# Optimization experiments

Measured on AMD Instinct MI355X. Metric: run time of the kernel, lower is better.

Reference implementation:

```python
import jax, jax.numpy as jnp
import numpy as np

DIM = 1024
NUM_HEADS = 16
DIM_HEAD = 64
POOL = 8  # int(sqrt(agent_num=64))
SCALE = DIM_HEAD ** -0.5


def setup_inputs() -> dict:
    key = jax.random.key(0)
    k1, k2, k3, k4 = jax.random.split(key, 4)
    inner = NUM_HEADS * DIM_HEAD
    x = jax.random.normal(k1, (4, 4096, DIM), dtype=jnp.float32)
    # qkv Linear (no bias): weight stored as (in, out) so forward is x @ Wqkv
    Wqkv = jax.random.normal(k2, (DIM, 3 * inner), dtype=jnp.float32) * (DIM ** -0.5)
    Wo = jax.random.normal(k3, (inner, DIM), dtype=jnp.float32) * (inner ** -0.5)
    bo = jax.random.normal(k4, (DIM,), dtype=jnp.float32) * 0.01
    return {"x": x, "Wqkv": Wqkv, "Wo": Wo, "bo": bo}


def reference(x, Wqkv, Wo, bo):
    b, t, _ = x.shape
    h, d = NUM_HEADS, DIM_HEAD
    qkv = x @ Wqkv                                   # [b, t, 3*h*d]
    qkv = qkv.reshape(b, t, 3, h, d)                 # split (qkv h d)
    qkv = jnp.transpose(qkv, (2, 0, 3, 1, 4))        # [3, b, h, t, d]
    q, k, v = qkv[0], qkv[1], qkv[2]
    # AdaptiveAvgPool2d((POOL, d)) on [b,h,t,d]: identity on d, mean-pool t -> POOL
    # (t divisible by POOL -> exact reshape+mean)
    agent = q.reshape(b, h, POOL, t // POOL, d).mean(axis=3)  # [b, h, P, d]
    # stage 1: agents attend over keys, aggregate values
    s1 = jnp.einsum('bhid,bhjd->bhij', agent * SCALE, k)      # [b, h, P, t]
    p1 = jax.nn.softmax(s1, axis=-1)
    v_agent = jnp.einsum('bhij,bhjd->bhid', p1, v)            # [b, h, P, d]
    # stage 2: queries attend over agent tokens
    s2 = jnp.einsum('bhid,bhjd->bhij', q * SCALE, agent)      # [b, h, t, P]
    p2 = jax.nn.softmax(s2, axis=-1)
    out = jnp.einsum('bhij,bhjd->bhid', p2, v_agent)          # [b, h, t, d]
    out = jnp.transpose(out, (0, 2, 1, 3)).reshape(b, t, h * d)
    return out @ Wo + bo
```

## Files before the change

kernel.cpp:

```cpp
#include <hip/hip_runtime.h>
#include <hip/hip_bf16.h>
#include <stdint.h>

typedef __bf16 bf16;
typedef __attribute__((ext_vector_type(8))) __bf16 bf16x8;
typedef __attribute__((ext_vector_type(4))) float f32x4;
typedef __attribute__((ext_vector_type(4))) unsigned int u32x4;

#define NH 16
#define DH 64
#define POOL 8
#define BATCH 4
#define SEQ 4096
#define DIMV 1024
#define QKV_N (3*DIMV)
#define M_TOTAL (BATCH*SEQ)
#define SCALE_F 0.125f
#define AGS_F (SCALE_F / 512.0f)
#define BH (BATCH*NH)
#define TCH 16
#define TCL (SEQ/TCH)
#define HP 128

#define AS1(p) ((const __attribute__((address_space(1))) void*)(p))
#define AS3(p) ((__attribute__((address_space(3))) void*)(p))
typedef const __attribute__((address_space(3))) char* lds_cp;

__global__ void prep(const float* __restrict__ x, bf16* __restrict__ xb,
                     const float* __restrict__ Wqkv, bf16* __restrict__ WqkvT,
                     const float* __restrict__ Wo, bf16* __restrict__ WoT) {
  __shared__ float tile[32][33];
  const int b = blockIdx.x;
  if (b < 8192) {
    size_t i = ((size_t)b * 256 + threadIdx.x) * 8;
    float4 f0 = *(const float4*)(x + i);
    float4 f1 = *(const float4*)(x + i + 4);
    bf16x8 o;
    o[0] = (bf16)f0.x; o[1] = (bf16)f0.y; o[2] = (bf16)f0.z; o[3] = (bf16)f0.w;
    o[4] = (bf16)f1.x; o[5] = (bf16)f1.y; o[6] = (bf16)f1.z; o[7] = (bf16)f1.w;
    *(bf16x8*)(xb + i) = o;
    return;
  }
  const float* in; bf16* out; int C, bx, by;
  if (b < 9216) { int bb = b - 8192; in = Wqkv; out = WqkvT; C = QKV_N; bx = 64 + (bb & 31); by = bb >> 5; }
  else          { int bb = b - 9216; in = Wo;   out = WoT;   C = DIMV;  bx = bb & 31;        by = bb >> 5; }
  const int R = DIMV;
  int c0 = bx * 32, r0 = by * 32;
  int tx = threadIdx.x & 31, ty = threadIdx.x >> 5;
  for (int i = ty; i < 32; i += 8)
    tile[i][tx] = in[(size_t)(r0 + i) * C + c0 + tx];
  __syncthreads();
  for (int i = ty; i < 32; i += 8)
    out[(size_t)(c0 + i) * R + r0 + tx] = (bf16)tile[tx][i];
}

__global__ void pool_x(const bf16* __restrict__ xb, float* __restrict__ xpool) {
  const int bid = blockIdx.x;
  const int bucket = bid >> 3, slice = bid & 7;
  const int b = bucket >> 3, p = bucket & 7;
  const int tid = threadIdx.x;
  const int co = tid & 127;
  const int r0 = tid >> 7;
  const bf16* src = xb + ((size_t)b * SEQ + p * 512 + slice * 64 + r0) * DIMV + co * 8;
  float a[8] = {};
  for (int r = 0; r < 64; r += 2) {
    bf16x8 v = *(const bf16x8*)(src + (size_t)r * DIMV);
#pragma unroll
    for (int e = 0; e < 8; ++e) a[e] += (float)v[e];
  }
  float* dst = xpool + (size_t)bucket * DIMV + co * 8;
#pragma unroll
  for (int e = 0; e < 8; ++e) atomicAdd(&dst[e], a[e]);
}

__global__ void agent_build(const float* __restrict__ xpool, const float* __restrict__ Wqkv,
                            float* __restrict__ agent_s) {
  __shared__ float xp[256];
  const int bid = blockIdx.x;
  const int bp = bid >> 2, cs = bid & 3;
  const int tid = threadIdx.x;
  xp[tid] = xpool[(size_t)bp * DIMV + cs * 256 + tid];
  __syncthreads();
  float acc[4] = {};
  const float* wbase = Wqkv + (size_t)(cs * 256) * QKV_N + tid * 4;
#pragma unroll 8
  for (int c = 0; c < 256; ++c) {
    float xv = xp[c];
    float4 wv = *(const float4*)(wbase + (size_t)c * QKV_N);
    acc[0] += xv * wv.x; acc[1] += xv * wv.y; acc[2] += xv * wv.z; acc[3] += xv * wv.w;
  }
  float* dst = agent_s + (size_t)bp * DIMV + tid * 4;
#pragma unroll
  for (int j = 0; j < 4; ++j) atomicAdd(&dst[j], acc[j]);
}

__global__ void w2cat_build(const float* __restrict__ agent_s, const float* __restrict__ Wqkv,
                            bf16* __restrict__ scw) {
  __shared__ float ag[8][64];
  const int bid = blockIdx.x;
  const int ct = bid & 3, qk = (bid >> 2) & 1, h = (bid >> 3) & 15, b = bid >> 7;
  const int tid = threadIdx.x;
  for (int i = tid; i < 512; i += 256)
    ag[i >> 6][i & 63] = agent_s[(size_t)(b * 8 + (i >> 6)) * DIMV + h * 64 + (i & 63)];
  __syncthreads();
  const int c = ct * 256 + tid;
  const float* wrow = Wqkv + (size_t)c * QKV_N + qk * 1024 + h * 64;
  float wv[64];
#pragma unroll
  for (int d4 = 0; d4 < 16; ++d4) {
    float4 w4 = *(const float4*)(wrow + d4 * 4);
    wv[d4 * 4] = w4.x; wv[d4 * 4 + 1] = w4.y; wv[d4 * 4 + 2] = w4.z; wv[d4 * 4 + 3] = w4.w;
  }
#pragma unroll
  for (int p = 0; p < 8; ++p) {
    float s = 0.f;
#pragma unroll
    for (int d = 0; d < 64; ++d) s += wv[d] * ag[p][d];
    scw[((size_t)b * 256 + qk * 128 + h * 8 + p) * DIMV + c] = (bf16)(s * AGS_F);
  }
}

__global__ __launch_bounds__(512, 2)
void vgemm(const bf16* __restrict__ A, const bf16* __restrict__ B,
           bf16* __restrict__ vOut) {
  constexpr int K1 = DIMV;
  constexpr int NI = K1 / 128;

  __shared__ __align__(16) bf16 LA[2][2][8192];
  __shared__ __align__(16) bf16 LB[2][2][8192];

  const int tid  = threadIdx.x;
  const int w    = tid >> 6;
  const int lane = tid & 63;
  const int wm = (w >> 2) * 128;
  const int wn = (w & 3) * 64;

  const int bid = blockIdx.x;
  const int swz = (bid & 7) * 32 + (bid >> 3);
  const int m0 = (swz >> 2) * 256;
  const int n0 = (swz & 3) * 256;

  const int rT  = tid >> 3;
  const int csT = (((tid & 7) ^ (rT & 7)) << 3);
  const bf16* Ag = A + (size_t)(m0 + rT) * K1 + csT;
  const bf16* Bg = B + (size_t)(n0 + rT) * K1 + csT;

  const int rA = lane & 15, C = lane >> 4, xr = rA & 7;
  const unsigned s0 = (unsigned)(((0 * 4 + C) ^ xr) << 4);
  const unsigned s1 = (unsigned)(((1 * 4 + C) ^ xr) << 4);
  const unsigned aoff = (unsigned)((wm + rA) << 7);
  const unsigned boff = (unsigned)((wn + rA) << 7);

  f32x4 acc[8][4] = {};
  u32x4 aR[4][2], bR[4][2];

#define STG(arr, Gp, half, kofs) do {                                         \
    const bf16* _s = (Gp) + (size_t)((half) * 128) * K1 + (kofs);             \
    char* _d = (char*)&arr[half][0] + (w << 10);                              \
    __builtin_amdgcn_global_load_lds(AS1(_s), AS3(_d), 16, 0, 0);             \
    __builtin_amdgcn_global_load_lds(AS1(_s + 64 * K1), AS3(_d + 8192), 16, 0, 0); \
  } while (0)

#define DSR0(d, p)    asm volatile("ds_read_b128 %0, %1" : "=v"(d) : "v"(p))
#define DSR(d, p, o)  asm volatile("ds_read_b128 %0, %1 offset:" o : "=v"(d) : "v"(p))

#define READS_A(LAb, qm) do {                                                 \
    lds_cp _p0 = (lds_cp)(const char*)&LAb[0][0] + aoff + s0 + (qm) * 8192;   \
    lds_cp _p1 = (lds_cp)(const char*)&LAb[0][0] + aoff + s1 + (qm) * 8192;   \
    DSR0(aR[0][0], _p0); DSR(aR[1][0], _p0, "2048");                          \
    DSR(aR[2][0], _p0, "4096"); DSR(aR[3][0], _p0, "6144");                   \
    DSR0(aR[0][1], _p1); DSR(aR[1][1], _p1, "2048");                          \
    DSR(aR[2][1], _p1, "4096"); DSR(aR[3][1], _p1, "6144");                   \
  } while (0)

#define READS_B01(LBb) do {                                                   \
    lds_cp _p0 = (lds_cp)(const char*)&LBb[0][0] + boff + s0;                 \
    lds_cp _p1 = (lds_cp)(const char*)&LBb[0][0] + boff + s1;                 \
    DSR0(bR[0][0], _p0); DSR(bR[1][0], _p0, "2048");                          \
    DSR0(bR[0][1], _p1); DSR(bR[1][1], _p1, "2048");                          \
  } while (0)

#define READS_B23(LBb) do {                                                   \
    lds_cp _p0 = (lds_cp)(const char*)&LBb[0][0] + boff + s0;                 \
    lds_cp _p1 = (lds_cp)(const char*)&LBb[0][0] + boff + s1;                 \
    DSR(bR[2][0], _p0, "4096"); DSR(bR[3][0], _p0, "6144");                   \
    DSR(bR[2][1], _p1, "4096"); DSR(bR[3][1], _p1, "6144");                   \
  } while (0)

#define WAITL8 do { asm volatile("s_waitcnt lgkmcnt(8)");                     \
                    __builtin_amdgcn_sched_barrier(0); } while (0)

#define MFMA_Q(qm, qn) do {                                                   \
    asm volatile("s_waitcnt lgkmcnt(0)");                                     \
    __builtin_amdgcn_sched_barrier(0);                                        \
    __builtin_amdgcn_s_setprio(1);                                            \
    _Pragma("unroll")                                                         \
    for (int il = 0; il < 4; ++il)                                            \
      _Pragma("unroll")                                                       \
      for (int jj = 0; jj < 2; ++jj) {                                        \
        f32x4& ac = acc[(qm) * 4 + il][(qn) * 2 + jj];                        \
        ac = __builtin_amdgcn_mfma_f32_16x16x32_bf16(                         \
            __builtin_bit_cast(bf16x8, aR[il][0]),                            \
            __builtin_bit_cast(bf16x8, bR[(qn) * 2 + jj][0]), ac, 0, 0, 0);   \
        ac = __builtin_amdgcn_mfma_f32_16x16x32_bf16(                         \
            __builtin_bit_cast(bf16x8, aR[il][1]),                            \
            __builtin_bit_cast(bf16x8, bR[(qn) * 2 + jj][1]), ac, 0, 0, 0);   \
      }                                                                       \
    __builtin_amdgcn_s_setprio(0);                                            \
    __builtin_amdgcn_sched_barrier(0);                                        \
  } while (0)

#define BAR __builtin_amdgcn_s_barrier()

  STG(LA[0], Ag, 0, 0); STG(LA[0], Ag, 1, 0);
  STG(LB[0], Bg, 0, 0); STG(LB[0], Bg, 1, 0);
  STG(LB[1], Bg, 0, 64); STG(LB[1], Bg, 1, 64);
  asm volatile("s_waitcnt vmcnt(4)");
  __builtin_amdgcn_sched_barrier(0);
  BAR;

  int kk = 0;
  for (int i = 0; i < NI - 1; ++i, kk += 128) {
    READS_A(LA[0], 0); READS_B01(LB[0]);
    STG(LA[1], Ag, 0, kk + 64);
    WAITL8;
    BAR; MFMA_Q(0, 0); BAR;
    READS_B23(LB[0]);
    STG(LA[1], Ag, 1, kk + 64);
    BAR; MFMA_Q(0, 1); BAR;
    READS_A(LA[0], 1);
    STG(LB[0], Bg, 0, kk + 128);
    BAR; MFMA_Q(1, 0); BAR;
    STG(LB[0], Bg, 1, kk + 128);
    BAR; MFMA_Q(1, 1);
    asm volatile("s_waitcnt vmcnt(4)");
    __builtin_amdgcn_sched_barrier(0);
    BAR;
    READS_A(LA[1], 0); READS_B01(LB[1]);
    STG(LA[0], Ag, 0, kk + 128);
    WAITL8;
    BAR; MFMA_Q(0, 0); BAR;
    READS_B23(LB[1]);
    STG(LA[0], Ag, 1, kk + 128);
    BAR; MFMA_Q(0, 1); BAR;
    READS_A(LA[1], 1);
    STG(LB[1], Bg, 0, kk + 192);
    BAR; MFMA_Q(1, 0); BAR;
    STG(LB[1], Bg, 1, kk + 192);
    BAR; MFMA_Q(1, 1);
    asm volatile("s_waitcnt vmcnt(4)");
    __builtin_amdgcn_sched_barrier(0);
    BAR;
  }
  READS_A(LA[0], 0); READS_B01(LB[0]);
  STG(LA[1], Ag, 0, kk + 64);
  WAITL8;
  BAR; MFMA_Q(0, 0); BAR;
  READS_B23(LB[0]);
  STG(LA[1], Ag, 1, kk + 64);
  BAR; MFMA_Q(0, 1); BAR;
  READS_A(LA[0], 1);
  BAR; MFMA_Q(1, 0); BAR;
  MFMA_Q(1, 1);
  asm volatile("s_waitcnt vmcnt(0)");
  __builtin_amdgcn_sched_barrier(0);
  BAR;
  READS_A(LA[1], 0); READS_B01(LB[1]);
  WAITL8;
  BAR; MFMA_Q(0, 0); BAR;
  READS_B23(LB[1]);
  BAR; MFMA_Q(0, 1); BAR;
  READS_A(LA[1], 1);
  BAR; MFMA_Q(1, 0); BAR;
  MFMA_Q(1, 1);

#undef STG
#undef DSR0
#undef DSR
#undef READS_A
#undef READS_B01
#undef READS_B23
#undef WAITL8
#undef MFMA_Q
#undef BAR

  const int cr = (lane >> 4) * 4;
  const int cc = lane & 15;
  const int ncol = n0 + wn;
  const int hh   = ncol >> 6;
  const int rowb = m0 + wm;
  const int bb_  = rowb >> 12;
  const int tb   = rowb & 4095;
  bf16* Cp = vOut + (size_t)(bb_ * NH + hh) * SEQ * DH;
#pragma unroll
  for (int i = 0; i < 8; ++i)
#pragma unroll
    for (int j = 0; j < 4; ++j)
#pragma unroll
      for (int r = 0; r < 4; ++r)
        Cp[(size_t)(tb + i * 16 + cr + r) * DH + (ncol & 63) + j * 16 + cc] = (bf16)acc[i][j][r];
}

__global__ __launch_bounds__(256)
void score_gemm(const bf16* __restrict__ A, const bf16* __restrict__ B,
                float* __restrict__ SC) {
  constexpr int K = DIMV;
  __shared__ bf16 As[128 * 32];
  __shared__ bf16 Bs[128 * 32];
  const int tid  = threadIdx.x;
  const int w    = tid >> 6;
  const int lane = tid & 63;
  const int m0 = blockIdx.y * 128, n0 = blockIdx.x * 128;
  const int wm = (w & 1) * 64, wn = (w >> 1) * 64;

  const bf16* Bb = B + (size_t)(m0 >> 12) * 256 * K;

  f32x4 acc[4][4] = {};

  const int g0  = w * 2;
  const int rig = lane >> 2;
  const int kcs = (lane & 3) ^ ((rig >> 1) & 3);
  const bf16* Ap0 = A + (size_t)(m0 + g0 * 16 + rig) * K + kcs * 8;
  const bf16* Ap1 = Ap0 + (size_t)16 * K;
  const bf16* Bp0 = Bb + (size_t)(n0 + g0 * 16 + rig) * K + kcs * 8;
  const bf16* Bp1 = Bp0 + (size_t)16 * K;
  bf16* AsW0 = As + g0 * 512;
  bf16* AsW1 = As + (g0 + 1) * 512;
  bf16* BsW0 = Bs + g0 * 512;
  bf16* BsW1 = Bs + (g0 + 1) * 512;

  for (int k0 = 0; k0 < K; k0 += 32) {
    __syncthreads();
    __builtin_amdgcn_global_load_lds(AS1(Ap0 + k0), AS3(AsW0), 16, 0, 0);
    __builtin_amdgcn_global_load_lds(AS1(Ap1 + k0), AS3(AsW1), 16, 0, 0);
    __builtin_amdgcn_global_load_lds(AS1(Bp0 + k0), AS3(BsW0), 16, 0, 0);
    __builtin_amdgcn_global_load_lds(AS1(Bp1 + k0), AS3(BsW1), 16, 0, 0);
    __syncthreads();

    bf16x8 a[4], b[4];
    const int C = lane >> 4;
#pragma unroll
    for (int i = 0; i < 4; ++i) {
      int ar = wm + i * 16 + (lane & 15);
      int sw = C ^ ((ar >> 1) & 3);
      a[i] = *(const bf16x8*)&As[ar * 32 + sw * 8];
    }
#pragma unroll
    for (int j = 0; j < 4; ++j) {
      int br = wn + j * 16 + (lane & 15);
      int sw = C ^ ((br >> 1) & 3);
      b[j] = *(const bf16x8*)&Bs[br * 32 + sw * 8];
    }
#pragma unroll
    for (int i = 0; i < 4; ++i)
#pragma unroll
      for (int j = 0; j < 4; ++j)
        acc[i][j] = __builtin_amdgcn_mfma_f32_16x16x32_bf16(a[i], b[j], acc[i][j], 0, 0, 0);
  }

  const int cr = (lane >> 4) * 4;
  const int cc = lane & 15;
#pragma unroll
  for (int i = 0; i < 4; ++i) {
#pragma unroll
    for (int j = 0; j < 4; ++j) {
      int col = n0 + wn + j * 16 + cc;
      int qk = col >> 7, h = (col >> 3) & 15, p = col & 7;
#pragma unroll
      for (int r = 0; r < 4; ++r) {
        int row = m0 + wm + i * 16 + cr + r;
        int b = row >> 12, t = row & 4095;
        SC[((size_t)(b * NH + h) * SEQ + t) * 16 + qk * 8 + p] = acc[i][j][r];
      }
    }
  }
}

__global__ __launch_bounds__(256)
void attn_mid(const float* __restrict__ SC, const bf16* __restrict__ v,
              bf16* __restrict__ P2,
              float* __restrict__ pm, float* __restrict__ pl,
              float* __restrict__ pva) {
  const int tc = blockIdx.x, bh = blockIdx.y;
  const int tid = threadIdx.x;
  const int t0 = tc * TCL;

  __shared__ float se[TCL][9];
  __shared__ float rm[4][8], rl[4][8];

  const float* scp = SC + ((size_t)bh * SEQ + t0 + tid) * 16;
  float4 sq0 = *(const float4*)(scp);
  float4 sq1 = *(const float4*)(scp + 4);
  float4 sk0 = *(const float4*)(scp + 8);
  float4 sk1 = *(const float4*)(scp + 12);
  float scq[8] = {sq0.x, sq0.y, sq0.z, sq0.w, sq1.x, sq1.y, sq1.z, sq1.w};
  float sck[8] = {sk0.x, sk0.y, sk0.z, sk0.w, sk1.x, sk1.y, sk1.z, sk1.w};

  {
    float m = scq[0];
#pragma unroll
    for (int p = 1; p < 8; ++p) m = fmaxf(m, scq[p]);
    float wsum = 0.f, wgt[8];
#pragma unroll
    for (int p = 0; p < 8; ++p) { wgt[p] = __expf(scq[p] - m); wsum += wgt[p]; }
    float inv = 1.0f / wsum;
    int b = bh >> 4, h = bh & 15;
    bf16x8 o8;
#pragma unroll
    for (int p = 0; p < 8; ++p) o8[p] = (bf16)(wgt[p] * inv);
    *(bf16x8*)&P2[((size_t)(b * SEQ + t0 + tid)) * HP + h * 8] = o8;
  }

  float mx[8];
#pragma unroll
  for (int p = 0; p < 8; ++p) mx[p] = sck[p];
#pragma unroll
  for (int o = 32; o; o >>= 1)
#pragma unroll
    for (int p = 0; p < 8; ++p) mx[p] = fmaxf(mx[p], __shfl_xor(mx[p], o));
  if ((tid & 63) == 0)
#pragma unroll
    for (int p = 0; p < 8; ++p) rm[tid >> 6][p] = mx[p];
  __syncthreads();
  float m[8];
#pragma unroll
  for (int p = 0; p < 8; ++p)
    m[p] = fmaxf(fmaxf(rm[0][p], rm[1][p]), fmaxf(rm[2][p], rm[3][p]));

  float sl[8];
#pragma unroll
  for (int p = 0; p < 8; ++p) {
    float e = __expf(sck[p] - m[p]);
    se[tid][p] = e;
    sl[p] = e;
  }
#pragma unroll
  for (int o = 32; o; o >>= 1)
#pragma unroll
    for (int p = 0; p < 8; ++p) sl[p] += __shfl_xor(sl[p], o);
  if ((tid & 63) == 0)
#pragma unroll
    for (int p = 0; p < 8; ++p) rl[tid >> 6][p] = sl[p];
  __syncthreads();
  if (tid < 8) {
    float l = rl[0][tid] + rl[1][tid] + rl[2][tid] + rl[3][tid];
    pm[(size_t)(bh * TCH + tc) * 8 + tid] = m[tid];
    pl[(size_t)(bh * TCH + tc) * 8 + tid] = l;
  }
  __syncthreads();

  const int lane = tid & 63;
  const int wv = tid >> 6;
  const int dg = lane & 7;
  const int to = lane >> 3;
  const int p0 = wv * 2;
  const bf16* vb = v + ((size_t)bh * SEQ + t0 + to) * DH + dg * 8;
  float a0[8] = {}, a1[8] = {};
  for (int tl = to; tl < TCL; tl += 8) {
    bf16x8 v8 = *(const bf16x8*)(vb + (size_t)(tl - to) * DH);
    float w0 = se[tl][p0];
    float w1 = se[tl][p0 + 1];
#pragma unroll
    for (int e = 0; e < 8; ++e) {
      float vf = (float)v8[e];
      a0[e] += w0 * vf;
      a1[e] += w1 * vf;
    }
  }
#pragma unroll
  for (int o = 8; o <= 32; o <<= 1) {
#pragma unroll
    for (int e = 0; e < 8; ++e) {
      a0[e] += __shfl_xor(a0[e], o);
      a1[e] += __shfl_xor(a1[e], o);
    }
  }
  if (to == 0) {
    float* o0 = pva + ((size_t)(bh * TCH + tc) * 8 + p0) * DH + dg * 8;
    float* o1 = o0 + DH;
#pragma unroll
    for (int e = 0; e < 8; ++e) { o0[e] = a0[e]; o1[e] = a1[e]; }
  }
}

__global__ void combine_vag(const float* __restrict__ pm, const float* __restrict__ pl,
                            const float* __restrict__ pva, float* __restrict__ vag) {
  int bh = blockIdx.x;
#pragma unroll
  for (int e = threadIdx.x; e < 512; e += 256) {
    int p = e >> 6, d = e & 63;
    float M = -1e30f;
#pragma unroll
    for (int tc = 0; tc < TCH; ++tc)
      M = fmaxf(M, pm[(size_t)(bh * TCH + tc) * 8 + p]);
    float L = 0.f, acc = 0.f;
#pragma unroll
    for (int tc = 0; tc < TCH; ++tc) {
      float w = __expf(pm[(size_t)(bh * TCH + tc) * 8 + p] - M);
      L   += w * pl[(size_t)(bh * TCH + tc) * 8 + p];
      acc += w * pva[((size_t)(bh * TCH + tc) * 8 + p) * DH + d];
    }
    vag[(size_t)bh * 512 + e] = acc / L;
  }
}

__global__ void w2_build(const float* __restrict__ vag, const bf16* __restrict__ WoT,
                         bf16* __restrict__ W2T) {
  int b = blockIdx.y;
  int n = blockIdx.x * 16 + (threadIdx.x & 15);
  int h = threadIdx.x >> 4;
  __shared__ float vg[128][65];
  for (int i = threadIdx.x; i < 128 * 64; i += 256)
    vg[i >> 6][i & 63] = vag[(size_t)b * 128 * 64 + i];
  __syncthreads();
  float acc[8] = {};
  const bf16* wrow = WoT + (size_t)n * DIMV + h * 64;
#pragma unroll
  for (int dv = 0; dv < 8; ++dv) {
    bf16x8 wv = *(const bf16x8*)(wrow + dv * 8);
#pragma unroll
    for (int e = 0; e < 8; ++e) {
      float wf = (float)wv[e];
      int d = dv * 8 + e;
#pragma unroll
      for (int p = 0; p < 8; ++p) acc[p] += vg[h * 8 + p][d] * wf;
    }
  }
  bf16x8 o;
#pragma unroll
  for (int p = 0; p < 8; ++p) o[p] = (bf16)acc[p];
  *(bf16x8*)&W2T[((size_t)b * DIMV + n) * HP + h * 8] = o;
}

__global__ __launch_bounds__(512, 2)
void gemm2_256(const bf16* __restrict__ A, const bf16* __restrict__ B,
               float* __restrict__ Out, const float* __restrict__ bias) {
  constexpr int K2 = HP;

  __shared__ __align__(16) bf16 LA[2][2][8192];
  __shared__ __align__(16) bf16 LB[2][2][8192];

  const int tid  = threadIdx.x;
  const int w    = tid >> 6;
  const int lane = tid & 63;
  const int wm = (w >> 2) * 128;
  const int wn = (w & 3) * 64;

  const int bid = blockIdx.x;
  const int swz = (bid & 7) * 32 + (bid >> 3);
  const int m0 = (swz >> 2) * 256;
  const int n0 = (swz & 3) * 256;

  const int rT  = tid >> 3;
  const int csT = (((tid & 7) ^ (rT & 7)) << 3);
  const bf16* Ag = A + (size_t)(m0 + rT) * K2 + csT;
  const bf16* Bg = B + ((size_t)(m0 >> 12) * DIMV + n0 + rT) * K2 + csT;

  const int rA = lane & 15, C = lane >> 4, xr = rA & 7;
  const unsigned s0 = (unsigned)(((0 * 4 + C) ^ xr) << 4);
  const unsigned s1 = (unsigned)(((1 * 4 + C) ^ xr) << 4);
  const unsigned aoff = (unsigned)((wm + rA) << 7);
  const unsigned boff = (unsigned)((wn + rA) << 7);

  f32x4 acc[8][4] = {};
  u32x4 aR[4][2], bR[4][2];

#define STG(arr, Gp, half, kofs) do {                                         \
    const bf16* _s = (Gp) + (size_t)((half) * 128) * K2 + (kofs);             \
    char* _d = (char*)&arr[half][0] + (w << 10);                              \
    __builtin_amdgcn_global_load_lds(AS1(_s), AS3(_d), 16, 0, 0);             \
    __builtin_amdgcn_global_load_lds(AS1(_s + 64 * K2), AS3(_d + 8192), 16, 0, 0); \
  } while (0)

#define DSR0(d, p)    asm volatile("ds_read_b128 %0, %1" : "=v"(d) : "v"(p))
#define DSR(d, p, o)  asm volatile("ds_read_b128 %0, %1 offset:" o : "=v"(d) : "v"(p))

#define READS_A(LAb, qm) do {                                                 \
    lds_cp _p0 = (lds_cp)(const char*)&LAb[0][0] + aoff + s0 + (qm) * 8192;   \
    lds_cp _p1 = (lds_cp)(const char*)&LAb[0][0] + aoff + s1 + (qm) * 8192;   \
    DSR0(aR[0][0], _p0); DSR(aR[1][0], _p0, "2048");                          \
    DSR(aR[2][0], _p0, "4096"); DSR(aR[3][0], _p0, "6144");                   \
    DSR0(aR[0][1], _p1); DSR(aR[1][1], _p1, "2048");                          \
    DSR(aR[2][1], _p1, "4096"); DSR(aR[3][1], _p1, "6144");                   \
  } while (0)

#define READS_B01(LBb) do {                                                   \
    lds_cp _p0 = (lds_cp)(const char*)&LBb[0][0] + boff + s0;                 \
    lds_cp _p1 = (lds_cp)(const char*)&LBb[0][0] + boff + s1;                 \
    DSR0(bR[0][0], _p0); DSR(bR[1][0], _p0, "2048");                          \
    DSR0(bR[0][1], _p1); DSR(bR[1][1], _p1, "2048");                          \
  } while (0)

#define READS_B23(LBb) do {                                                   \
    lds_cp _p0 = (lds_cp)(const char*)&LBb[0][0] + boff + s0;                 \
    lds_cp _p1 = (lds_cp)(const char*)&LBb[0][0] + boff + s1;                 \
    DSR(bR[2][0], _p0, "4096"); DSR(bR[3][0], _p0, "6144");                   \
    DSR(bR[2][1], _p1, "4096"); DSR(bR[3][1], _p1, "6144");                   \
  } while (0)

#define WAITL8 do { asm volatile("s_waitcnt lgkmcnt(8)");                     \
                    __builtin_amdgcn_sched_barrier(0); } while (0)

#define MFMA_Q(qm, qn) do {                                                   \
    asm volatile("s_waitcnt lgkmcnt(0)");                                     \
    __builtin_amdgcn_sched_barrier(0);                                        \
    __builtin_amdgcn_s_setprio(1);                                            \
    _Pragma("unroll")                                                         \
    for (int il = 0; il < 4; ++il)                                            \
      _Pragma("unroll")                                                       \
      for (int jj = 0; jj < 2; ++jj) {                                        \
        f32x4& ac = acc[(qm) * 4 + il][(qn) * 2 + jj];                        \
        ac = __builtin_amdgcn_mfma_f32_16x16x32_bf16(                         \
            __builtin_bit_cast(bf16x8, aR[il][0]),                            \
            __builtin_bit_cast(bf16x8, bR[(qn) * 2 + jj][0]), ac, 0, 0, 0);   \
        ac = __builtin_amdgcn_mfma_f32_16x16x32_bf16(                         \
            __builtin_bit_cast(bf16x8, aR[il][1]),                            \
            __builtin_bit_cast(bf16x8, bR[(qn) * 2 + jj][1]), ac, 0, 0, 0);   \
      }                                                                       \
    __builtin_amdgcn_s_setprio(0);                                            \
    __builtin_amdgcn_sched_barrier(0);                                        \
  } while (0)

#define BAR __builtin_amdgcn_s_barrier()

  STG(LA[0], Ag, 0, 0); STG(LA[0], Ag, 1, 0);
  STG(LB[0], Bg, 0, 0); STG(LB[0], Bg, 1, 0);
  STG(LB[1], Bg, 0, 64); STG(LB[1], Bg, 1, 64);
  asm volatile("s_waitcnt vmcnt(4)");
  __builtin_amdgcn_sched_barrier(0);
  BAR;

  READS_A(LA[0], 0); READS_B01(LB[0]);
  STG(LA[1], Ag, 0, 64);
  WAITL8;
  BAR; MFMA_Q(0, 0); BAR;
  READS_B23(LB[0]);
  STG(LA[1], Ag, 1, 64);
  BAR; MFMA_Q(0, 1); BAR;
  READS_A(LA[0], 1);
  BAR; MFMA_Q(1, 0); BAR;
  MFMA_Q(1, 1);
  asm volatile("s_waitcnt vmcnt(0)");
  __builtin_amdgcn_sched_barrier(0);
  BAR;
  READS_A(LA[1], 0); READS_B01(LB[1]);
  WAITL8;
  BAR; MFMA_Q(0, 0); BAR;
  READS_B23(LB[1]);
  BAR; MFMA_Q(0, 1); BAR;
  READS_A(LA[1], 1);
  BAR; MFMA_Q(1, 0); BAR;
  MFMA_Q(1, 1);

#undef STG
#undef DSR0
#undef DSR
#undef READS_A
#undef READS_B01
#undef READS_B23
#undef WAITL8
#undef MFMA_Q
#undef BAR

  const int cr = (lane >> 4) * 4;
  const int cc = lane & 15;
  const int rowb = m0 + wm;
  float bb4[4];
#pragma unroll
  for (int j = 0; j < 4; ++j) bb4[j] = bias[n0 + wn + j * 16 + cc];
#pragma unroll
  for (int i = 0; i < 8; ++i)
#pragma unroll
    for (int j = 0; j < 4; ++j) {
      const int col = n0 + wn + j * 16 + cc;
#pragma unroll
      for (int r = 0; r < 4; ++r)
        Out[(size_t)(rowb + i * 16 + cr + r) * DIMV + col] = acc[i][j][r] + bb4[j];
    }
}

extern "C" void kernel_launch(void* const* d_in, const int* in_sizes, int n_in,
                              void* d_out, int out_size, void* d_ws, size_t ws_size,
                              hipStream_t stream) {
  const float* x    = (const float*)d_in[0];
  const float* Wqkv = (const float*)d_in[1];
  const float* Wo   = (const float*)d_in[2];
  const float* bo   = (const float*)d_in[3];
  float* out = (float*)d_out;

  char* ws = (char*)d_ws;
  bf16*  WqkvT  = (bf16*)ws;                                 ws += (size_t)QKV_N * DIMV * 2;
  bf16*  WoT    = (bf16*)ws;                                 ws += (size_t)DIMV * DIMV * 2;
  bf16*  vpl    = (bf16*)ws;                                 ws += (size_t)BH * SEQ * DH * 2;
  char*  wsu    = ws;                                        ws += (size_t)M_TOTAL * DIMV * 2;
  bf16*  xb     = (bf16*)wsu;
  bf16*  P2     = (bf16*)wsu;
  bf16*  W2T    = (bf16*)(wsu + (size_t)M_TOTAL * HP * 2);
  float* SC     = (float*)ws;                                ws += (size_t)BH * SEQ * 16 * 4;
  bf16*  scw    = (bf16*)ws;                                 ws += (size_t)BATCH * 256 * DIMV * 2;
  float* xpool  = (float*)ws;                                ws += 32 * DIMV * 4;
  float* agent_s= (float*)ws;                                ws += 32 * DIMV * 4;
  float* pm     = (float*)ws;                                ws += BH * TCH * 8 * 4;
  float* pl     = (float*)ws;                                ws += BH * TCH * 8 * 4;
  float* pva    = (float*)ws;                                ws += (size_t)BH * TCH * 8 * DH * 4;
  float* vag    = (float*)ws;                                ws += 512 * 64 * 4;

  hipMemsetAsync(xpool, 0, 32 * DIMV * 4, stream);
  hipMemsetAsync(agent_s, 0, 32 * DIMV * 4, stream);

  prep<<<10240, 256, 0, stream>>>(x, xb, Wqkv, WqkvT, Wo, WoT);

  pool_x<<<256, 256, 0, stream>>>(xb, xpool);
  agent_build<<<128, 256, 0, stream>>>(xpool, Wqkv, agent_s);
  w2cat_build<<<512, 256, 0, stream>>>(agent_s, Wqkv, scw);

  vgemm<<<256, 512, 0, stream>>>(xb, WqkvT + (size_t)2048 * DIMV, vpl);

  score_gemm<<<dim3(2, 128), 256, 0, stream>>>(xb, scw, SC);

  attn_mid<<<dim3(TCH, BH), 256, 0, stream>>>(SC, vpl, P2, pm, pl, pva);

  combine_vag<<<BH, 256, 0, stream>>>(pm, pl, pva, vag);
  w2_build<<<dim3(DIMV / 16, BATCH), 256, 0, stream>>>(vag, WoT, W2T);

  gemm2_256<<<256, 512, 0, stream>>>(P2, W2T, out, bo);
}
```

Baseline: 306.9 us.

## Merge score GEMM into V GEMM launch and store scores plane-major

Removes the separate score_gemm kernel and folds its work into the V projection GEMM kernel as 64 extra 256x256 tiles in one 320-block launch, using the faster pipelined MFMA path for the score GEMM. Score outputs move to a plane-major layout ([16][BH*SEQ]) so the GEMM writes float4 stores along t and attn_mid reads coalesced per-plane values. This saves one launch and its tail, and speeds up the score computation. In exchange, block work becomes mixed, and the attn_mid loads turn into 16 strided scalar reads per thread.

```diff
diff --git a/kernel.cpp b/kernel.cpp
--- a/kernel.cpp
+++ b/kernel.cpp
@@ -21,6 +21,7 @@
 #define TCH 16
 #define TCL (SEQ/TCH)
 #define HP 128
+#define SCPL ((size_t)BH*SEQ)
 
 #define AS1(p) ((const __attribute__((address_space(1))) void*)(p))
 #define AS3(p) ((__attribute__((address_space(3))) void*)(p))
@@ -121,8 +122,9 @@
 }
 
 __global__ __launch_bounds__(512, 2)
-void vgemm(const bf16* __restrict__ A, const bf16* __restrict__ B,
-           bf16* __restrict__ vOut) {
+void vscore_gemm(const bf16* __restrict__ A, const bf16* __restrict__ Bv,
+                 const bf16* __restrict__ scw,
+                 bf16* __restrict__ vOut, float* __restrict__ SC) {
   constexpr int K1 = DIMV;
   constexpr int NI = K1 / 128;
 
@@ -136,14 +138,23 @@
   const int wn = (w & 3) * 64;
 
   const int bid = blockIdx.x;
-  const int swz = (bid & 7) * 32 + (bid >> 3);
-  const int m0 = (swz >> 2) * 256;
-  const int n0 = (swz & 3) * 256;
+  const int swz = (bid & 7) * 40 + (bid >> 3);
+  const bool isScore = swz < 64;
+  int m0, n0;
+  const bf16* Bg0;
+  if (isScore) {
+    m0 = swz * 256; n0 = 0;
+    Bg0 = scw + (size_t)(m0 >> 12) * 256 * K1;
+  } else {
+    const int vi = swz - 64;
+    m0 = (vi >> 2) * 256; n0 = (vi & 3) * 256;
+    Bg0 = Bv;
+  }
 
   const int rT  = tid >> 3;
   const int csT = (((tid & 7) ^ (rT & 7)) << 3);
   const bf16* Ag = A + (size_t)(m0 + rT) * K1 + csT;
-  const bf16* Bg = B + (size_t)(n0 + rT) * K1 + csT;
+  const bf16* Bg = Bg0 + (size_t)(n0 + rT) * K1 + csT;
 
   const int rA = lane & 15, C = lane >> 4, xr = rA & 7;
   const unsigned s0 = (unsigned)(((0 * 4 + C) ^ xr) << 4);
@@ -286,93 +297,32 @@
 
   const int cr = (lane >> 4) * 4;
   const int cc = lane & 15;
-  const int ncol = n0 + wn;
-  const int hh   = ncol >> 6;
   const int rowb = m0 + wm;
   const int bb_  = rowb >> 12;
   const int tb   = rowb & 4095;
-  bf16* Cp = vOut + (size_t)(bb_ * NH + hh) * SEQ * DH;
-#pragma unroll
-  for (int i = 0; i < 8; ++i)
-#pragma unroll
-    for (int j = 0; j < 4; ++j)
-#pragma unroll
-      for (int r = 0; r < 4; ++r)
-        Cp[(size_t)(tb + i * 16 + cr + r) * DH + (ncol & 63) + j * 16 + cc] = (bf16)acc[i][j][r];
-}
-
-__global__ __launch_bounds__(256)
-void score_gemm(const bf16* __restrict__ A, const bf16* __restrict__ B,
-                float* __restrict__ SC) {
-  constexpr int K = DIMV;
-  __shared__ bf16 As[128 * 32];
-  __shared__ bf16 Bs[128 * 32];
-  const int tid  = threadIdx.x;
-  const int w    = tid >> 6;
-  const int lane = tid & 63;
-  const int m0 = blockIdx.y * 128, n0 = blockIdx.x * 128;
-  const int wm = (w & 1) * 64, wn = (w >> 1) * 64;
-
-  const bf16* Bb = B + (size_t)(m0 >> 12) * 256 * K;
-
-  f32x4 acc[4][4] = {};
-
-  const int g0  = w * 2;
-  const int rig = lane >> 2;
-  const int kcs = (lane & 3) ^ ((rig >> 1) & 3);
-  const bf16* Ap0 = A + (size_t)(m0 + g0 * 16 + rig) * K + kcs * 8;
-  const bf16* Ap1 = Ap0 + (size_t)16 * K;
-  const bf16* Bp0 = Bb + (size_t)(n0 + g0 * 16 + rig) * K + kcs * 8;
-  const bf16* Bp1 = Bp0 + (size_t)16 * K;
-  bf16* AsW0 = As + g0 * 512;
-  bf16* AsW1 = As + (g0 + 1) * 512;
-  bf16* BsW0 = Bs + g0 * 512;
-  bf16* BsW1 = Bs + (g0 + 1) * 512;
-
-  for (int k0 = 0; k0 < K; k0 += 32) {
-    __syncthreads();
-    __builtin_amdgcn_global_load_lds(AS1(Ap0 + k0), AS3(AsW0), 16, 0, 0);
-    __builtin_amdgcn_global_load_lds(AS1(Ap1 + k0), AS3(AsW1), 16, 0, 0);
-    __builtin_amdgcn_global_load_lds(AS1(Bp0 + k0), AS3(BsW0), 16, 0, 0);
-    __builtin_amdgcn_global_load_lds(AS1(Bp1 + k0), AS3(BsW1), 16, 0, 0);
-    __syncthreads();
-
-    bf16x8 a[4], b[4];
-    const int C = lane >> 4;
-#pragma unroll
-    for (int i = 0; i < 4; ++i) {
-      int ar = wm + i * 16 + (lane & 15);
-      int sw = C ^ ((ar >> 1) & 3);
-      a[i] = *(const bf16x8*)&As[ar * 32 + sw * 8];
-    }
-#pragma unroll
-    for (int j = 0; j < 4; ++j) {
-      int br = wn + j * 16 + (lane & 15);
-      int sw = C ^ ((br >> 1) & 3);
-      b[j] = *(const bf16x8*)&Bs[br * 32 + sw * 8];
-    }
-#pragma unroll
-    for (int i = 0; i < 4; ++i)
+
+  if (isScore) {
+#pragma unroll
+    for (int i = 0; i < 8; ++i)
+#pragma unroll
+      for (int j = 0; j < 4; ++j) {
+        const int col = wn + j * 16 + cc;
+        const int plane = ((col >> 7) << 3) | (col & 7);
+        const int h = (col >> 3) & 15;
+        float4 st = {acc[i][j][0], acc[i][j][1], acc[i][j][2], acc[i][j][3]};
+        *(float4*)&SC[(size_t)plane * SCPL + ((size_t)(bb_ * NH + h)) * SEQ + tb + i * 16 + cr] = st;
+      }
+  } else {
+    const int ncol = n0 + wn;
+    const int hh   = ncol >> 6;
+    bf16* Cp = vOut + (size_t)(bb_ * NH + hh) * SEQ * DH;
+#pragma unroll
+    for (int i = 0; i < 8; ++i)
 #pragma unroll
       for (int j = 0; j < 4; ++j)
-        acc[i][j] = __builtin_amdgcn_mfma_f32_16x16x32_bf16(a[i], b[j], acc[i][j], 0, 0, 0);
-  }
-
-  const int cr = (lane >> 4) * 4;
-  const int cc = lane & 15;
-#pragma unroll
-  for (int i = 0; i < 4; ++i) {
-#pragma unroll
-    for (int j = 0; j < 4; ++j) {
-      int col = n0 + wn + j * 16 + cc;
-      int qk = col >> 7, h = (col >> 3) & 15, p = col & 7;
-#pragma unroll
-      for (int r = 0; r < 4; ++r) {
-        int row = m0 + wm + i * 16 + cr + r;
-        int b = row >> 12, t = row & 4095;
-        SC[((size_t)(b * NH + h) * SEQ + t) * 16 + qk * 8 + p] = acc[i][j][r];
-      }
-    }
+#pragma unroll
+        for (int r = 0; r < 4; ++r)
+          Cp[(size_t)(tb + i * 16 + cr + r) * DH + (ncol & 63) + j * 16 + cc] = (bf16)acc[i][j][r];
   }
 }
 
@@ -388,13 +338,13 @@
   __shared__ float se[TCL][9];
   __shared__ float rm[4][8], rl[4][8];
 
-  const float* scp = SC + ((size_t)bh * SEQ + t0 + tid) * 16;
-  float4 sq0 = *(const float4*)(scp);
-  float4 sq1 = *(const float4*)(scp + 4);
-  float4 sk0 = *(const float4*)(scp + 8);
-  float4 sk1 = *(const float4*)(scp + 12);
-  float scq[8] = {sq0.x, sq0.y, sq0.z, sq0.w, sq1.x, sq1.y, sq1.z, sq1.w};
-  float sck[8] = {sk0.x, sk0.y, sk0.z, sk0.w, sk1.x, sk1.y, sk1.z, sk1.w};
+  const float* scb = SC + (size_t)bh * SEQ + t0 + tid;
+  float scq[8], sck[8];
+#pragma unroll
+  for (int p = 0; p < 8; ++p) {
+    scq[p] = scb[(size_t)p * SCPL];
+    sck[p] = scb[(size_t)(8 + p) * SCPL];
+  }
 
   {
     float m = scq[0];
@@ -696,7 +646,7 @@
   bf16*  xb     = (bf16*)wsu;
   bf16*  P2     = (bf16*)wsu;
   bf16*  W2T    = (bf16*)(wsu + (size_t)M_TOTAL * HP * 2);
-  float* SC     = (float*)ws;                                ws += (size_t)BH * SEQ * 16 * 4;
+  float* SC     = (float*)ws;                                ws += (size_t)16 * SCPL * 4;
   bf16*  scw    = (bf16*)ws;                                 ws += (size_t)BATCH * 256 * DIMV * 2;
   float* xpool  = (float*)ws;                                ws += 32 * DIMV * 4;
   float* agent_s= (float*)ws;                                ws += 32 * DIMV * 4;
@@ -714,9 +664,7 @@
   agent_build<<<128, 256, 0, stream>>>(xpool, Wqkv, agent_s);
   w2cat_build<<<512, 256, 0, stream>>>(agent_s, Wqkv, scw);
 
-  vgemm<<<256, 512, 0, stream>>>(xb, WqkvT + (size_t)2048 * DIMV, vpl);
-
-  score_gemm<<<dim3(2, 128), 256, 0, stream>>>(xb, scw, SC);
+  vscore_gemm<<<320, 512, 0, stream>>>(xb, WqkvT + (size_t)2048 * DIMV, scw, vpl, SC);
 
   attn_mid<<<dim3(TCH, BH), 256, 0, stream>>>(SC, vpl, P2, pm, pl, pva);
 
```

New measurement: 302.9 us. About the same (-1.3%).
